# Kernel tuning notes

Measured on AMD Instinct MI355X. Metric: run time of the kernel, lower is better.

Reference implementation:

```python
import jax, jax.numpy as jnp
import numpy as np

B, H, N, D, A = 96, 100, 128, 768, 256  # batch, max_history_num, news_num, news_embedding_dim, attention_dim


def setup_inputs() -> dict:
    key = jax.random.key(0)
    ks = jax.random.split(key, 6)
    w = lambda k, shape: jax.random.normal(k, shape, jnp.float32) * 0.02
    return {
        "history_embedding": jax.random.normal(ks[0], (B, H, D), jnp.float32),
        "candidate_news_representation": jax.random.normal(ks[1], (B, N, D), jnp.float32),
        "W_l": w(ks[2], (D, D)),              # SAGEConv lin_l (neighbor) weight
        "b_l": jnp.zeros((D,), jnp.float32),  # SAGEConv lin_l bias
        "W_r": w(ks[3], (D, D)),              # SAGEConv lin_r (root) weight, bias=False
        "W_K": w(ks[4], (A, D)),              # K Linear, bias=False
        "W_Q": w(ks[5], (A, D)),              # Q Linear, bias=True
        "b_Q": jnp.zeros((A,), jnp.float32),
    }


def reference(history_embedding, candidate_news_representation, W_l, b_l, W_r, W_K, W_Q, b_Q):
    b, h, d = history_embedding.shape
    n = candidate_news_representation.shape[1]
    a_dim = W_K.shape[0]

    # --- GraphSAGE (1 layer SAGEConv, mean aggr, PyG node_dim=-2) ---
    # edge_index: src = user rows 0..b-1 (indexing the history dim!), dst = 0..h-1.
    # Every dst h receives all srcs 0..b-1, so the mean-aggregated neighbor feature is
    # mean over the first b history slots, identical for every h.
    neigh = jnp.mean(history_embedding[:, :b, :], axis=1)  # [b, d]
    gcn = (
        jnp.einsum("bhd,ed->bhe", history_embedding, W_r)
        + (neigh @ W_l.T + b_l)[:, None, :]
    )  # [b, h, d]

    # --- K/Q attention pooling over history ---
    user_rep = gcn[:, 0, :]                                  # [b, d] (gcn_feature[:, :1, :])
    K = jnp.einsum("bhd,ad->bha", gcn, W_K)                  # [b, h, A]
    Q = user_rep @ W_Q.T + b_Q                               # [b, A]
    scores = jnp.einsum("bha,ba->bh", K, Q) / jnp.sqrt(jnp.float32(a_dim))
    alpha = jax.nn.softmax(scores, axis=1)                   # [b, h]
    out = jnp.einsum("bh,bhd->bd", alpha, gcn)               # [b, d]

    # In torch, news_rep/user_rep2 are expand()ed over news_num with identical content,
    # so the per-candidate outputs are all equal: broadcast instead of recomputing.
    return jnp.broadcast_to(out[:, None, :], (b, n, d))
```

## Files before the change

### kernel.cpp

```cpp
#include <hip/hip_runtime.h>
#include <hip/hip_bf16.h>

#define BB 96
#define HH 100
#define NN 128
#define DD 768
#define AA 256

#define WSLAB 196608
#define WSLAB4 49152

static __device__ __forceinline__ float dot4(float4 a, float4 b) {
  return a.x * b.x + a.y * b.y + a.z * b.z + a.w * b.w;
}

__global__ void __launch_bounds__(256)
k_prep(const float* __restrict__ Wr, const float* __restrict__ WK,
       const float* __restrict__ hist,
       float* __restrict__ MTp, float* __restrict__ neighp) {
  int bid = blockIdx.x, tid = threadIdx.x;
  if (bid < 768) {
    __shared__ float sL[32][33];
    __shared__ float sR[32][33];
    int s = bid / 192;
    int t = bid % 192;
    int d0 = (t % 24) * 32, a0 = (t / 24) * 32;
    int tx = tid & 31, ty = tid >> 5;
    float acc[4] = {0.f, 0.f, 0.f, 0.f};
    int ebase = s * 192;
    for (int e0 = ebase; e0 < ebase + 192; e0 += 32) {
#pragma unroll
      for (int k = 0; k < 4; ++k) {
        sL[ty + 8 * k][tx] = WK[(size_t)(a0 + ty + 8 * k) * DD + e0 + tx];
        sR[ty + 8 * k][tx] = Wr[(size_t)(e0 + ty + 8 * k) * DD + d0 + tx];
      }
      __syncthreads();
#pragma unroll 8
      for (int e = 0; e < 32; ++e) {
        float w = sR[e][tx];
#pragma unroll
        for (int k = 0; k < 4; ++k) acc[k] += sL[ty + 8 * k][e] * w;
      }
      __syncthreads();
    }
#pragma unroll
    for (int k = 0; k < 4; ++k) sL[ty + 8 * k][tx] = acc[k];
    __syncthreads();
    float* MTs = MTp + (size_t)s * WSLAB;
#pragma unroll
    for (int k = 0; k < 4; ++k)
      MTs[(size_t)(d0 + ty + 8 * k) * AA + a0 + tx] = sL[tx][ty + 8 * k];
  } else {
    int id = bid - 768;
    int b = id % BB, hg = id / BB;
    if (tid < 192) {
      const float* hb = hist + (size_t)b * HH * DD + (size_t)hg * 24 * DD + tid * 4;
      float4 a0 = make_float4(0.f, 0.f, 0.f, 0.f);
      float4 a1 = make_float4(0.f, 0.f, 0.f, 0.f);
#pragma unroll
      for (int h = 0; h < 24; h += 2) {
        float4 x = *(const float4*)(hb + (size_t)h * DD);
        float4 y = *(const float4*)(hb + (size_t)(h + 1) * DD);
        a0.x += x.x; a0.y += x.y; a0.z += x.z; a0.w += x.w;
        a1.x += y.x; a1.y += y.y; a1.z += y.z; a1.w += y.w;
      }
      float4 m = make_float4(a0.x + a1.x, a0.y + a1.y, a0.z + a1.z, a0.w + a1.w);
      *(float4*)(neighp + ((size_t)hg * BB + b) * DD + tid * 4) = m;
    }
  }
}

__global__ void k_nl_u0(const float* __restrict__ neighp, const float* __restrict__ hist,
                        const float* __restrict__ Wl, const float* __restrict__ bl,
                        const float* __restrict__ Wr,
                        float* __restrict__ nl, float* __restrict__ u0) {
  int e0 = blockIdx.x * 32;
  int b0 = blockIdx.y * 3;
  int lane = threadIdx.x & 63, wave = threadIdx.x >> 6;
  float4 xn[3][3], xh[3][3];
#pragma unroll
  for (int bi = 0; bi < 3; ++bi) {
    int b = b0 + bi;
#pragma unroll
    for (int jj = 0; jj < 3; ++jj) {
      int idx = lane + 64 * jj;
      float4 s = make_float4(0.f, 0.f, 0.f, 0.f);
#pragma unroll
      for (int g = 0; g < 4; ++g) {
        float4 x = ((const float4*)(neighp + ((size_t)g * BB + b) * DD))[idx];
        s.x += x.x; s.y += x.y; s.z += x.z; s.w += x.w;
      }
      xn[bi][jj] = make_float4(s.x * (1.f / 96.f), s.y * (1.f / 96.f),
                               s.z * (1.f / 96.f), s.w * (1.f / 96.f));
      xh[bi][jj] = ((const float4*)(hist + (size_t)b * HH * DD))[idx];
    }
  }
  for (int i = 0; i < 8; ++i) {
    int e = e0 + wave * 8 + i;
    const float4* wl4 = (const float4*)(Wl + (size_t)e * DD);
    const float4* wr4 = (const float4*)(Wr + (size_t)e * DD);
    float pl[3] = {0.f, 0.f, 0.f}, pr[3] = {0.f, 0.f, 0.f};
#pragma unroll
    for (int jj = 0; jj < 3; ++jj) {
      float4 wl = wl4[lane + 64 * jj];
      float4 wr = wr4[lane + 64 * jj];
#pragma unroll
      for (int bi = 0; bi < 3; ++bi) {
        pl[bi] += dot4(wl, xn[bi][jj]);
        pr[bi] += dot4(wr, xh[bi][jj]);
      }
    }
#pragma unroll
    for (int bi = 0; bi < 3; ++bi) {
      float pp = pl[bi], qq = pr[bi];
      for (int off = 32; off; off >>= 1) {
        pp += __shfl_down(pp, off, 64);
        qq += __shfl_down(qq, off, 64);
      }
      if (lane == 0) {
        float nle = pp + bl[e];
        nl[(size_t)(b0 + bi) * DD + e] = nle;
        u0[(size_t)(b0 + bi) * DD + e] = qq + nle;
      }
    }
  }
}

__global__ void __launch_bounds__(256)
k_q(const float* __restrict__ u0, const float* __restrict__ WQ,
    const float* __restrict__ bQ, const float* __restrict__ MTp,
    float* __restrict__ Qm, float* __restrict__ MT) {
  int bid = blockIdx.x, tid = threadIdx.x;
  if (bid < 256) {
    int a0 = (bid & 7) * 32;
    int b0 = (bid >> 3) * 3;
    int lane = tid & 63, wave = tid >> 6;
    float4 x[3][3];
#pragma unroll
    for (int bi = 0; bi < 3; ++bi)
#pragma unroll
      for (int jj = 0; jj < 3; ++jj)
        x[bi][jj] = ((const float4*)(u0 + (size_t)(b0 + bi) * DD))[lane + 64 * jj];
    for (int i = 0; i < 8; ++i) {
      int a = a0 + wave * 8 + i;
      const float4* w4 = (const float4*)(WQ + (size_t)a * DD);
      float p[3] = {0.f, 0.f, 0.f};
#pragma unroll
      for (int jj = 0; jj < 3; ++jj) {
        float4 w = w4[lane + 64 * jj];
#pragma unroll
        for (int bi = 0; bi < 3; ++bi) p[bi] += dot4(w, x[bi][jj]);
      }
#pragma unroll
      for (int bi = 0; bi < 3; ++bi) {
        float pp = p[bi];
        for (int off = 32; off; off >>= 1) pp += __shfl_down(pp, off, 64);
        if (lane == 0) Qm[(size_t)(b0 + bi) * AA + a] = pp + bQ[a];
      }
    }
  } else {
    int i4 = (bid - 256) * 256 + tid;
    const float4* p = (const float4*)MTp;
    float4 a = p[i4], b = p[WSLAB4 + i4], c = p[2 * WSLAB4 + i4], d = p[3 * WSLAB4 + i4];
    ((float4*)MT)[i4] = make_float4(a.x + b.x + c.x + d.x, a.y + b.y + c.y + d.y,
                                    a.z + b.z + c.z + d.z, a.w + b.w + c.w + d.w);
  }
}

__global__ void k_v(const float* __restrict__ Qm, const float* __restrict__ MT,
                    float* __restrict__ vv) {
  int d0 = blockIdx.x * 32;
  int b0 = blockIdx.y * 3;
  int lane = threadIdx.x & 63, wave = threadIdx.x >> 6;
  float4 x[3];
#pragma unroll
  for (int bi = 0; bi < 3; ++bi)
    x[bi] = ((const float4*)(Qm + (size_t)(b0 + bi) * AA))[lane];
  for (int i = 0; i < 8; ++i) {
    int d = d0 + wave * 8 + i;
    float4 w = ((const float4*)(MT + (size_t)d * AA))[lane];
    float p[3];
#pragma unroll
    for (int bi = 0; bi < 3; ++bi) p[bi] = dot4(w, x[bi]);
#pragma unroll
    for (int bi = 0; bi < 3; ++bi) {
      float pp = p[bi];
      for (int off = 32; off; off >>= 1) pp += __shfl_down(pp, off, 64);
      if (lane == 0) vv[(size_t)(b0 + bi) * DD + d] = pp * (1.f / 16.f);
    }
  }
}

__global__ void k_scores(const float* __restrict__ hist, const float* __restrict__ vv,
                         float* __restrict__ sc) {
  int b = blockIdx.x, hg = blockIdx.y;
  int lane = threadIdx.x & 63, wave = threadIdx.x >> 6;
  float4 v[3];
  const float4* vb = (const float4*)(vv + (size_t)b * DD);
#pragma unroll
  for (int jj = 0; jj < 3; ++jj) v[jj] = vb[lane + 64 * jj];
  const float* hb = hist + (size_t)b * HH * DD;
  for (int i = 0; i < 5; ++i) {
    int h = hg * 20 + wave * 5 + i;
    const float4* r = (const float4*)(hb + (size_t)h * DD);
    float p = 0.f;
#pragma unroll
    for (int jj = 0; jj < 3; ++jj) p += dot4(r[lane + 64 * jj], v[jj]);
    for (int off = 32; off; off >>= 1) p += __shfl_down(p, off, 64);
    if (lane == 0) sc[b * 128 + h] = p;
  }
}

__global__ void __launch_bounds__(256)
k_wsum(const float* __restrict__ hist, const float* __restrict__ sc,
       float* __restrict__ wsum) {
  int b = blockIdx.x;
  int es = blockIdx.y;
  int tid = threadIdx.x, lane = tid & 63, wave = tid >> 6;
  __shared__ float sal[HH];
  __shared__ float psum[4][64];
  if (tid < HH) sal[tid] = sc[b * 128 + tid];
  __syncthreads();
  if (wave == 0) {
    float x0 = (lane < HH) ? sal[lane] : -1e30f;
    float x1 = (lane + 64 < HH) ? sal[lane + 64] : -1e30f;
    float m = fmaxf(x0, x1);
    for (int off = 32; off; off >>= 1) m = fmaxf(m, __shfl_xor(m, off, 64));
    float e0 = (lane < HH) ? __expf(x0 - m) : 0.f;
    float e1 = (lane + 64 < HH) ? __expf(x1 - m) : 0.f;
    float s = e0 + e1;
    for (int off = 32; off; off >>= 1) s += __shfl_xor(s, off, 64);
    float inv = 1.f / s;
    if (lane < HH) sal[lane] = e0 * inv;
    if (lane + 64 < HH) sal[lane + 64] = e1 * inv;
  }
  __syncthreads();
  int e = es * 64 + lane;
  const float* hb = hist + (size_t)b * HH * DD + e;
  int h0 = wave * 25;
  float acc = 0.f;
#pragma unroll
  for (int i = 0; i < 25; i += 5) {
    float v0 = hb[(size_t)(h0 + i + 0) * DD];
    float v1 = hb[(size_t)(h0 + i + 1) * DD];
    float v2 = hb[(size_t)(h0 + i + 2) * DD];
    float v3 = hb[(size_t)(h0 + i + 3) * DD];
    float v4 = hb[(size_t)(h0 + i + 4) * DD];
    acc += sal[h0 + i + 0] * v0 + sal[h0 + i + 1] * v1 + sal[h0 + i + 2] * v2 +
           sal[h0 + i + 3] * v3 + sal[h0 + i + 4] * v4;
  }
  psum[wave][lane] = acc;
  __syncthreads();
  if (tid < 64) {
    float s = psum[0][tid] + psum[1][tid] + psum[2][tid] + psum[3][tid];
    wsum[(size_t)b * DD + es * 64 + tid] = s;
  }
}

__global__ void k_orow_write(const float* __restrict__ wsum, const float* __restrict__ Wr,
                             const float* __restrict__ nl, float* __restrict__ out) {
  int d0 = blockIdx.x * 32;
  int b0 = blockIdx.y * 3;
  int lane = threadIdx.x & 63, wave = threadIdx.x >> 6;
  __shared__ __align__(16) float s_o[3][32];
  float4 x[3][3];
#pragma unroll
  for (int bi = 0; bi < 3; ++bi)
#pragma unroll
    for (int jj = 0; jj < 3; ++jj)
      x[bi][jj] = ((const float4*)(wsum + (size_t)(b0 + bi) * DD))[lane + 64 * jj];
  for (int i = 0; i < 8; ++i) {
    int d = d0 + wave * 8 + i;
    const float4* w4 = (const float4*)(Wr + (size_t)d * DD);
    float p[3] = {0.f, 0.f, 0.f};
#pragma unroll
    for (int jj = 0; jj < 3; ++jj) {
      float4 w = w4[lane + 64 * jj];
#pragma unroll
      for (int bi = 0; bi < 3; ++bi) p[bi] += dot4(w, x[bi][jj]);
    }
#pragma unroll
    for (int bi = 0; bi < 3; ++bi) {
      float pp = p[bi];
      for (int off = 32; off; off >>= 1) pp += __shfl_down(pp, off, 64);
      if (lane == 0)
        s_o[bi][wave * 8 + i] = pp + nl[(size_t)(b0 + bi) * DD + d];
    }
  }
  __syncthreads();
  float4* out4 = (float4*)out;
  int d4 = d0 >> 2;
#pragma unroll
  for (int k = 0; k < 12; ++k) {
    int g = threadIdx.x + (k << 8);
    int seg = g >> 3, off = g & 7;
    int bi = seg >> 7, n = seg & 127;
    float4 val = *(const float4*)&s_o[bi][off * 4];
    out4[((size_t)(b0 + bi) * NN + n) * (DD / 4) + d4 + off] = val;
  }
}

extern "C" void kernel_launch(void* const* d_in, const int* in_sizes, int n_in,
                              void* d_out, int out_size, void* d_ws, size_t ws_size,
                              hipStream_t stream) {
  const float *hist = nullptr, *Wl = nullptr, *Wr = nullptr, *WK = nullptr,
              *WQ = nullptr, *bl = nullptr, *bQ = nullptr;
  int seenDxD = 0, seenAxD = 0;
  for (int i = 0; i < n_in; ++i) {
    int s = in_sizes[i];
    const float* p = (const float*)d_in[i];
    if (s == BB * HH * DD) hist = p;
    else if (s == BB * NN * DD) {  }
    else if (s == DD * DD) { if (seenDxD++ == 0) Wl = p; else Wr = p; }
    else if (s == AA * DD) { if (seenAxD++ == 0) WK = p; else WQ = p; }
    else if (s == DD) bl = p;
    else if (s == AA) bQ = p;
  }

  float* ws = (float*)d_ws;
  float* MTp    = ws + 0;
  float* MT     = ws + 786432;
  float* neighp = ws + 983040;
  float* nl     = ws + 1277952;
  float* u0     = ws + 1351680;
  float* Qm     = ws + 1425408;
  float* vv     = ws + 1449984;
  float* sc     = ws + 1523712;
  float* wsum   = ws + 1536000;
  float* out = (float*)d_out;

  k_prep      <<<dim3(1152),   dim3(256), 0, stream>>>(Wr, WK, hist, MTp, neighp);
  k_nl_u0     <<<dim3(24, 32), dim3(256), 0, stream>>>(neighp, hist, Wl, bl, Wr, nl, u0);
  k_q         <<<dim3(448),    dim3(256), 0, stream>>>(u0, WQ, bQ, MTp, Qm, MT);
  k_v         <<<dim3(24, 32), dim3(256), 0, stream>>>(Qm, MT, vv);
  k_scores    <<<dim3(96, 5),  dim3(256), 0, stream>>>(hist, vv, sc);
  k_wsum      <<<dim3(96, 12), dim3(256), 0, stream>>>(hist, sc, wsum);
  k_orow_write<<<dim3(24, 32), dim3(256), 0, stream>>>(wsum, Wr, nl, out);
}
```

Baseline: 87.43 us.

## Precompute combined MT·WQ matrix to remove Q stage and merge kernels

Instead of computing Q = u0·WQ^T + bQ and then v = MT·Q, the code builds G = MT·WQ (768x768) plus a bias vector cv = MT·bQ. These are computed in one merged launch alongside the nl/u0 projection, and k_v then applies G directly to u0. This drops one serialized kernel launch and the intermediate Q and MT buffers. In exchange it adds a 768x768x256 GEMM and makes k_v read a 768-wide G instead of a 256-wide MT.

```diff
diff --git a/kernel.cpp b/kernel.cpp
--- a/kernel.cpp
+++ b/kernel.cpp
@@ -8,7 +8,6 @@
 #define AA 256
 
 #define WSLAB 196608
-#define WSLAB4 49152
 
 static __device__ __forceinline__ float dot4(float4 a, float4 b) {
   return a.x * b.x + a.y * b.y + a.z * b.z + a.w * b.w;
@@ -70,123 +69,140 @@
   }
 }
 
-__global__ void k_nl_u0(const float* __restrict__ neighp, const float* __restrict__ hist,
-                        const float* __restrict__ Wl, const float* __restrict__ bl,
-                        const float* __restrict__ Wr,
-                        float* __restrict__ nl, float* __restrict__ u0) {
-  int e0 = blockIdx.x * 32;
-  int b0 = blockIdx.y * 3;
-  int lane = threadIdx.x & 63, wave = threadIdx.x >> 6;
-  float4 xn[3][3], xh[3][3];
-#pragma unroll
-  for (int bi = 0; bi < 3; ++bi) {
-    int b = b0 + bi;
-#pragma unroll
-    for (int jj = 0; jj < 3; ++jj) {
-      int idx = lane + 64 * jj;
-      float4 s = make_float4(0.f, 0.f, 0.f, 0.f);
-#pragma unroll
-      for (int g = 0; g < 4; ++g) {
-        float4 x = ((const float4*)(neighp + ((size_t)g * BB + b) * DD))[idx];
-        s.x += x.x; s.y += x.y; s.z += x.z; s.w += x.w;
-      }
-      xn[bi][jj] = make_float4(s.x * (1.f / 96.f), s.y * (1.f / 96.f),
-                               s.z * (1.f / 96.f), s.w * (1.f / 96.f));
-      xh[bi][jj] = ((const float4*)(hist + (size_t)b * HH * DD))[idx];
-    }
-  }
-  for (int i = 0; i < 8; ++i) {
-    int e = e0 + wave * 8 + i;
-    const float4* wl4 = (const float4*)(Wl + (size_t)e * DD);
-    const float4* wr4 = (const float4*)(Wr + (size_t)e * DD);
-    float pl[3] = {0.f, 0.f, 0.f}, pr[3] = {0.f, 0.f, 0.f};
-#pragma unroll
-    for (int jj = 0; jj < 3; ++jj) {
-      float4 wl = wl4[lane + 64 * jj];
-      float4 wr = wr4[lane + 64 * jj];
+__global__ void __launch_bounds__(256)
+k_mid(const float* __restrict__ MTp, const float* __restrict__ WQ,
+      const float* __restrict__ bQ, const float* __restrict__ neighp,
+      const float* __restrict__ hist, const float* __restrict__ Wl,
+      const float* __restrict__ bl, const float* __restrict__ Wr,
+      float* __restrict__ G, float* __restrict__ nl, float* __restrict__ u0,
+      float* __restrict__ cv) {
+  int bid = blockIdx.x, tid = threadIdx.x;
+  if (bid < 576) {
+    __shared__ float sA[32][33];
+    __shared__ float sB[32][33];
+    int d1_0 = (bid % 24) * 32, d2_0 = (bid / 24) * 32;
+    int tx = tid & 31, ty = tid >> 5;
+    float acc[4] = {0.f, 0.f, 0.f, 0.f};
+    for (int a0 = 0; a0 < AA; a0 += 32) {
+#pragma unroll
+      for (int k = 0; k < 4; ++k) {
+        size_t rMT = (size_t)(d2_0 + ty + 8 * k) * AA + a0 + tx;
+        sA[ty + 8 * k][tx] = MTp[rMT] + MTp[WSLAB + rMT] +
+                             MTp[2 * WSLAB + rMT] + MTp[3 * WSLAB + rMT];
+        sB[ty + 8 * k][tx] = WQ[(size_t)(a0 + ty + 8 * k) * DD + d1_0 + tx];
+      }
+      __syncthreads();
+#pragma unroll 8
+      for (int a = 0; a < 32; ++a) {
+        float wb = sB[a][tx];
+#pragma unroll
+        for (int k = 0; k < 4; ++k) acc[k] += sA[ty + 8 * k][a] * wb;
+      }
+      __syncthreads();
+    }
+#pragma unroll
+    for (int k = 0; k < 4; ++k)
+      G[(size_t)(d2_0 + ty + 8 * k) * DD + d1_0 + tx] = acc[k];
+  } else if (bid < 1344) {
+    int id = bid - 576;
+    int e0 = (id % 24) * 32;
+    int b0 = (id / 24) * 3;
+    int lane = tid & 63, wave = tid >> 6;
+    float4 xn[3][3], xh[3][3];
+#pragma unroll
+    for (int bi = 0; bi < 3; ++bi) {
+      int b = b0 + bi;
+#pragma unroll
+      for (int jj = 0; jj < 3; ++jj) {
+        int idx = lane + 64 * jj;
+        float4 s = make_float4(0.f, 0.f, 0.f, 0.f);
+#pragma unroll
+        for (int g = 0; g < 4; ++g) {
+          float4 x = ((const float4*)(neighp + ((size_t)g * BB + b) * DD))[idx];
+          s.x += x.x; s.y += x.y; s.z += x.z; s.w += x.w;
+        }
+        xn[bi][jj] = make_float4(s.x * (1.f / 96.f), s.y * (1.f / 96.f),
+                                 s.z * (1.f / 96.f), s.w * (1.f / 96.f));
+        xh[bi][jj] = ((const float4*)(hist + (size_t)b * HH * DD))[idx];
+      }
+    }
+    for (int i = 0; i < 8; ++i) {
+      int e = e0 + wave * 8 + i;
+      const float4* wl4 = (const float4*)(Wl + (size_t)e * DD);
+      const float4* wr4 = (const float4*)(Wr + (size_t)e * DD);
+      float pl[3] = {0.f, 0.f, 0.f}, pr[3] = {0.f, 0.f, 0.f};
+#pragma unroll
+      for (int jj = 0; jj < 3; ++jj) {
+        float4 wl = wl4[lane + 64 * jj];
+        float4 wr = wr4[lane + 64 * jj];
+#pragma unroll
+        for (int bi = 0; bi < 3; ++bi) {
+          pl[bi] += dot4(wl, xn[bi][jj]);
+          pr[bi] += dot4(wr, xh[bi][jj]);
+        }
+      }
 #pragma unroll
       for (int bi = 0; bi < 3; ++bi) {
-        pl[bi] += dot4(wl, xn[bi][jj]);
-        pr[bi] += dot4(wr, xh[bi][jj]);
-      }
-    }
-#pragma unroll
-    for (int bi = 0; bi < 3; ++bi) {
-      float pp = pl[bi], qq = pr[bi];
-      for (int off = 32; off; off >>= 1) {
-        pp += __shfl_down(pp, off, 64);
-        qq += __shfl_down(qq, off, 64);
-      }
-      if (lane == 0) {
-        float nle = pp + bl[e];
-        nl[(size_t)(b0 + bi) * DD + e] = nle;
-        u0[(size_t)(b0 + bi) * DD + e] = qq + nle;
-      }
-    }
-  }
-}
-
-__global__ void __launch_bounds__(256)
-k_q(const float* __restrict__ u0, const float* __restrict__ WQ,
-    const float* __restrict__ bQ, const float* __restrict__ MTp,
-    float* __restrict__ Qm, float* __restrict__ MT) {
-  int bid = blockIdx.x, tid = threadIdx.x;
-  if (bid < 256) {
-    int a0 = (bid & 7) * 32;
-    int b0 = (bid >> 3) * 3;
+        float pp = pl[bi], qq = pr[bi];
+        for (int off = 32; off; off >>= 1) {
+          pp += __shfl_down(pp, off, 64);
+          qq += __shfl_down(qq, off, 64);
+        }
+        if (lane == 0) {
+          float nle = pp + bl[e];
+          nl[(size_t)(b0 + bi) * DD + e] = nle;
+          u0[(size_t)(b0 + bi) * DD + e] = qq + nle;
+        }
+      }
+    }
+  } else {
+    int d0 = (bid - 1344) * 32;
     int lane = tid & 63, wave = tid >> 6;
-    float4 x[3][3];
-#pragma unroll
-    for (int bi = 0; bi < 3; ++bi)
-#pragma unroll
-      for (int jj = 0; jj < 3; ++jj)
-        x[bi][jj] = ((const float4*)(u0 + (size_t)(b0 + bi) * DD))[lane + 64 * jj];
+    float4 x = ((const float4*)bQ)[lane];
     for (int i = 0; i < 8; ++i) {
-      int a = a0 + wave * 8 + i;
-      const float4* w4 = (const float4*)(WQ + (size_t)a * DD);
-      float p[3] = {0.f, 0.f, 0.f};
-#pragma unroll
-      for (int jj = 0; jj < 3; ++jj) {
-        float4 w = w4[lane + 64 * jj];
-#pragma unroll
-        for (int bi = 0; bi < 3; ++bi) p[bi] += dot4(w, x[bi][jj]);
-      }
-#pragma unroll
-      for (int bi = 0; bi < 3; ++bi) {
-        float pp = p[bi];
-        for (int off = 32; off; off >>= 1) pp += __shfl_down(pp, off, 64);
-        if (lane == 0) Qm[(size_t)(b0 + bi) * AA + a] = pp + bQ[a];
-      }
-    }
-  } else {
-    int i4 = (bid - 256) * 256 + tid;
-    const float4* p = (const float4*)MTp;
-    float4 a = p[i4], b = p[WSLAB4 + i4], c = p[2 * WSLAB4 + i4], d = p[3 * WSLAB4 + i4];
-    ((float4*)MT)[i4] = make_float4(a.x + b.x + c.x + d.x, a.y + b.y + c.y + d.y,
-                                    a.z + b.z + c.z + d.z, a.w + b.w + c.w + d.w);
-  }
-}
-
-__global__ void k_v(const float* __restrict__ Qm, const float* __restrict__ MT,
-                    float* __restrict__ vv) {
+      int d = d0 + wave * 8 + i;
+      size_t r4 = ((size_t)d * AA) / 4 + lane;
+      const float4* p0 = (const float4*)MTp;
+      float4 w0 = p0[r4];
+      float4 w1 = p0[WSLAB / 4 + r4];
+      float4 w2 = p0[2 * (WSLAB / 4) + r4];
+      float4 w3 = p0[3 * (WSLAB / 4) + r4];
+      float4 w = make_float4(w0.x + w1.x + w2.x + w3.x, w0.y + w1.y + w2.y + w3.y,
+                             w0.z + w1.z + w2.z + w3.z, w0.w + w1.w + w2.w + w3.w);
+      float p = dot4(w, x);
+      for (int off = 32; off; off >>= 1) p += __shfl_down(p, off, 64);
+      if (lane == 0) cv[d] = p;
+    }
+  }
+}
+
+__global__ void k_v(const float* __restrict__ u0, const float* __restrict__ G,
+                    const float* __restrict__ cv, float* __restrict__ vv) {
   int d0 = blockIdx.x * 32;
   int b0 = blockIdx.y * 3;
   int lane = threadIdx.x & 63, wave = threadIdx.x >> 6;
-  float4 x[3];
+  float4 x[3][3];
 #pragma unroll
   for (int bi = 0; bi < 3; ++bi)
-    x[bi] = ((const float4*)(Qm + (size_t)(b0 + bi) * AA))[lane];
+#pragma unroll
+    for (int jj = 0; jj < 3; ++jj)
+      x[bi][jj] = ((const float4*)(u0 + (size_t)(b0 + bi) * DD))[lane + 64 * jj];
   for (int i = 0; i < 8; ++i) {
     int d = d0 + wave * 8 + i;
-    float4 w = ((const float4*)(MT + (size_t)d * AA))[lane];
-    float p[3];
-#pragma unroll
-    for (int bi = 0; bi < 3; ++bi) p[bi] = dot4(w, x[bi]);
+    const float4* g4 = (const float4*)(G + (size_t)d * DD);
+    float p[3] = {0.f, 0.f, 0.f};
+#pragma unroll
+    for (int jj = 0; jj < 3; ++jj) {
+      float4 w = g4[lane + 64 * jj];
+#pragma unroll
+      for (int bi = 0; bi < 3; ++bi) p[bi] += dot4(w, x[bi][jj]);
+    }
 #pragma unroll
     for (int bi = 0; bi < 3; ++bi) {
       float pp = p[bi];
       for (int off = 32; off; off >>= 1) pp += __shfl_down(pp, off, 64);
-      if (lane == 0) vv[(size_t)(b0 + bi) * DD + d] = pp * (1.f / 16.f);
+      if (lane == 0)
+        vv[(size_t)(b0 + bi) * DD + d] = (pp + cv[d]) * (1.f / 16.f);
     }
   }
 }
@@ -319,20 +335,20 @@
 
   float* ws = (float*)d_ws;
   float* MTp    = ws + 0;
-  float* MT     = ws + 786432;
-  float* neighp = ws + 983040;
-  float* nl     = ws + 1277952;
-  float* u0     = ws + 1351680;
-  float* Qm     = ws + 1425408;
-  float* vv     = ws + 1449984;
-  float* sc     = ws + 1523712;
-  float* wsum   = ws + 1536000;
+  float* G      = ws + 786432;
+  float* neighp = ws + 1376256;
+  float* nl     = ws + 1671168;
+  float* u0     = ws + 1744896;
+  float* cv     = ws + 1818624;
+  float* vv     = ws + 1819648;
+  float* sc     = ws + 1893376;
+  float* wsum   = ws + 1905664;
   float* out = (float*)d_out;
 
   k_prep      <<<dim3(1152),   dim3(256), 0, stream>>>(Wr, WK, hist, MTp, neighp);
-  k_nl_u0     <<<dim3(24, 32), dim3(256), 0, stream>>>(neighp, hist, Wl, bl, Wr, nl, u0);
-  k_q         <<<dim3(448),    dim3(256), 0, stream>>>(u0, WQ, bQ, MTp, Qm, MT);
-  k_v         <<<dim3(24, 32), dim3(256), 0, stream>>>(Qm, MT, vv);
+  k_mid       <<<dim3(1368),   dim3(256), 0, stream>>>(MTp, WQ, bQ, neighp, hist,
+                                                       Wl, bl, Wr, G, nl, u0, cv);
+  k_v         <<<dim3(24, 32), dim3(256), 0, stream>>>(u0, G, cv, vv);
   k_scores    <<<dim3(96, 5),  dim3(256), 0, stream>>>(hist, vv, sc);
   k_wsum      <<<dim3(96, 12), dim3(256), 0, stream>>>(hist, sc, wsum);
   k_orow_write<<<dim3(24, 32), dim3(256), 0, stream>>>(wsum, Wr, nl, out);
```

Result: slower. 94.79 us (+8.4%).
